# Optimization experiments

Hardware: AMD Instinct MI355X
Metric: run time of the kernel (lower is better)

## Reference

```python
import jax, jax.numpy as jnp
import numpy as np

B, N, D, H = 8, 2048, 512, 8  # batch, seq (incl. CLS), emb_dim, heads


def setup_inputs() -> dict:
    key = jax.random.key(0)
    kx, km, k1, k2, k3, k4 = jax.random.split(key, 6)
    x = jax.random.normal(kx, (B, N, D), dtype=jnp.float32)
    # mask covers the N-1 non-CLS tokens; forward pads a leading True for CLS
    mask = jax.random.bernoulli(km, p=0.9, shape=(B, N - 1))
    s = 0.02
    Wqkv = jax.random.normal(k1, (D, 3 * D), dtype=jnp.float32) * s
    bqkv = jax.random.normal(k2, (3 * D,), dtype=jnp.float32) * s
    Wout = jax.random.normal(k3, (D, D), dtype=jnp.float32) * s
    bout = jax.random.normal(k4, (D,), dtype=jnp.float32) * s
    return {"x": x, "mask": mask, "Wqkv": Wqkv, "bqkv": bqkv,
            "Wout": Wout, "bout": bout, "num_heads": H}


def reference(x, mask, Wqkv, bqkv, Wout, bout, num_heads):
    b, n, d = x.shape
    h = num_heads
    dh = d // h
    scale = d ** (-0.5)  # NOTE: module scales by emb_dim^-0.5, not head_dim^-0.5

    qkv = x @ Wqkv + bqkv                      # [b, n, 3d]
    q, k, v = jnp.split(qkv, 3, axis=-1)
    def to_heads(t):
        return t.reshape(b, n, h, dh).transpose(0, 2, 1, 3)  # [b, h, n, dh]
    q, k, v = map(to_heads, (q, k, v))

    scores = jnp.einsum('bhqd,bhkd->bhqk', q, k) * scale     # [b, h, n, n]

    # pad leading True for CLS token, then outer-product pair mask
    m = jnp.pad(mask, ((0, 0), (1, 0)), constant_values=True)  # [b, n]
    pair = m[:, None, :, None] & m[:, None, None, :]           # [b, 1, n, n]
    neg = jnp.asarray(-1e9, dtype=scores.dtype)  # finite stand-in for -inf (avoids NaN rows)
    scores = jnp.where(pair, scores, neg)

    attn = jax.nn.softmax(scores, axis=-1)
    out = jnp.einsum('bhqk,bhkd->bhqd', attn, v)               # [b, h, n, dh]
    out = out.transpose(0, 2, 1, 3).reshape(b, n, d)
    return out @ Wout + bout
```

## Files before the change

### kernel.cpp

```cpp
#include <hip/hip_runtime.h>
#include <math.h>

#define BB  8
#define SEQ 2048
#define EMB 512
#define NH  8
#define DH  64
#define NBH (BB * NH)
#define MROWS (BB * SEQ)
#define QKV_ELEMS ((size_t)NBH * SEQ * DH)
#define MASK_ELEMS (BB * (SEQ - 1))
#define QSCALE 0.06375871307545f

typedef __attribute__((ext_vector_type(8))) short short8;
typedef __attribute__((ext_vector_type(4))) float float4e;
typedef unsigned short ushort_t;

static __device__ inline unsigned short f2bf(float f) {
    unsigned int u = __float_as_uint(f);
    unsigned int r = (u + 0x7fffu + ((u >> 16) & 1u)) >> 16;
    return (unsigned short)r;
}

static __device__ inline float bf2f(unsigned short h) {
    return __uint_as_float((unsigned int)h << 16);
}

static __device__ inline void gl_lds16(const unsigned short* g, unsigned short* l) {
    __builtin_amdgcn_global_load_lds(
        (const __attribute__((address_space(1))) void*)g,
        (__attribute__((address_space(3))) void*)l, 16, 0, 0);
}

#define PREP_CONV   8192
#define PREP_MASK   (PREP_CONV + 64)
#define PREP_WQ     (PREP_MASK + (1536 / 32) * (EMB / 32))
#define PREP_TOTAL  (PREP_WQ + (EMB / 32) * (EMB / 32))

__global__ __launch_bounds__(256) void prep(const float* __restrict__ x,
                                            const void* __restrict__ mraw,
                                            const float* __restrict__ Wqkv,
                                            const float* __restrict__ Wout,
                                            ushort_t* __restrict__ xb,
                                            ushort_t* __restrict__ pmh,
                                            ushort_t* __restrict__ wqt,
                                            ushort_t* __restrict__ wot) {
    __shared__ float T[32][33];
    __shared__ int flag;
    const int bid = blockIdx.x;
    const int tid = threadIdx.x;

    if (bid < PREP_CONV) {
        const size_t i = ((size_t)bid * 256 + tid) * 4;
        float4 v = *(const float4*)&x[i];
        ushort4 o;
        o.x = f2bf(v.x); o.y = f2bf(v.y); o.z = f2bf(v.z); o.w = f2bf(v.w);
        *(ushort4*)&xb[i] = o;
    } else if (bid < PREP_MASK) {
        if (tid == 0) flag = 0;
        __syncthreads();
        const unsigned int* mi = (const unsigned int*)mraw;
        int local = 0;
        for (int i = tid; i < MASK_ELEMS / 4; i += 256) {
            if (mi[i] > 1u) local = 1;
        }
        if (local) flag = 1;
        __syncthreads();
        const int isbyte = flag;
        const unsigned char* mb = (const unsigned char*)mraw;
        const int* m32 = (const int*)mraw;
        const int i = (bid - PREP_CONV) * 256 + tid;
        const int b = i >> 11, n = i & (SEQ - 1);
        int v;
        if (n == 0) v = 1;
        else {
            const int src = b * (SEQ - 1) + n - 1;
            v = isbyte ? (int)mb[src] : (m32[src] != 0 ? 1 : 0);
        }
        pmh[i] = v ? 0x3F80 : 0;
    } else {
        const float* src;
        ushort_t* dst;
        int N, idx;
        if (bid < PREP_WQ) {
            src = Wqkv; dst = wqt; N = 1536; idx = bid - PREP_MASK;
        } else {
            src = Wout; dst = wot; N = EMB; idx = bid - PREP_WQ;
        }
        const int nb = N / 32;
        const int n0 = (idx % nb) * 32;
        const int k0 = (idx / nb) * 32;
        {
            const int r = tid >> 3, c4 = (tid & 7) * 4;
            *(float4*)&T[r][c4] = *(const float4*)&src[(size_t)(k0 + r) * N + n0 + c4];
        }
        __syncthreads();
        const int n = tid >> 3, k4 = (tid & 7) * 4;
        ushort4 hv;
        hv.x = f2bf(T[k4 + 0][n]);
        hv.y = f2bf(T[k4 + 1][n]);
        hv.z = f2bf(T[k4 + 2][n]);
        hv.w = f2bf(T[k4 + 3][n]);
        *(ushort4*)&dst[(size_t)(n0 + n) * EMB + k0 + k4] = hv;
    }
}

__global__ __launch_bounds__(256) void qkv_mfma(const ushort_t* __restrict__ xb,
                                                const ushort_t* __restrict__ wt,
                                                const float* __restrict__ bias,
                                                ushort_t* __restrict__ qb,
                                                ushort_t* __restrict__ kb,
                                                ushort_t* __restrict__ vt) {
    __shared__ __align__(16) ushort_t As[128 * 32];
    __shared__ __align__(16) ushort_t Bs[128 * 32];
    const int tid  = threadIdx.x;
    const int w    = tid >> 6;
    const int lane = tid & 63;
    const int l16  = lane & 15;
    const int quad = lane >> 4;
    const int wq   = w >> 1;
    const int wn   = w & 1;
    const int row0 = blockIdx.y * 128;
    const int col0 = blockIdx.x * 128;

    float4e acc[4][4];
    #pragma unroll
    for (int i = 0; i < 4; ++i)
        #pragma unroll
        for (int j = 0; j < 4; ++j) acc[i][j] = (float4e){0.f, 0.f, 0.f, 0.f};

    const int srow = tid >> 2;
    const int csrc = (tid & 3) ^ (srow & 3);

    for (int k0 = 0; k0 < EMB; k0 += 32) {
        #pragma unroll
        for (int s = 0; s < 2; ++s) {
            const int row = s * 64 + srow;
            gl_lds16(xb + (size_t)(row0 + row) * EMB + k0 + csrc * 8,
                     As + s * 2048 + w * 512);
            gl_lds16(wt + (size_t)(col0 + row) * EMB + k0 + csrc * 8,
                     Bs + s * 2048 + w * 512);
        }
        __syncthreads();
        short8 af[4], bf[4];
        #pragma unroll
        for (int mt = 0; mt < 4; ++mt) {
            const int rm = wq * 64 + mt * 16 + l16;
            af[mt] = *(const short8*)(As + rm * 32 + ((quad ^ (rm & 3)) * 8));
        }
        #pragma unroll
        for (int nt = 0; nt < 4; ++nt) {
            const int rn = wn * 64 + nt * 16 + l16;
            bf[nt] = *(const short8*)(Bs + rn * 32 + ((quad ^ (rn & 3)) * 8));
        }
        #pragma unroll
        for (int mt = 0; mt < 4; ++mt)
            #pragma unroll
            for (int nt = 0; nt < 4; ++nt)
                acc[mt][nt] = __builtin_amdgcn_mfma_f32_16x16x32_bf16(af[mt], bf[nt], acc[mt][nt], 0, 0, 0);
        __syncthreads();
    }

    #pragma unroll
    for (int nt = 0; nt < 4; ++nt) {
        const int cb    = col0 + wn * 64 + nt * 16;
        const int which = cb >> 9;
        const int h     = (cb >> 6) & 7;
        const int dcol  = (cb & 63) + l16;
        const float bz  = bias[cb + l16];
        if (which == 2) {
            #pragma unroll
            for (int mt = 0; mt < 4; ++mt) {
                const int rg = row0 + wq * 64 + mt * 16 + quad * 4;
                const int b = rg >> 11, n = rg & (SEQ - 1);
                ushort4 ov;
                ov.x = f2bf(acc[mt][nt][0] + bz);
                ov.y = f2bf(acc[mt][nt][1] + bz);
                ov.z = f2bf(acc[mt][nt][2] + bz);
                ov.w = f2bf(acc[mt][nt][3] + bz);
                *(ushort4*)&vt[((size_t)(b * NH + h) * DH + dcol) * SEQ + n] = ov;
            }
        } else {
            ushort_t* base = (which == 0) ? qb : kb;
            const float sc = (which == 0) ? QSCALE : 1.0f;
            #pragma unroll
            for (int mt = 0; mt < 4; ++mt) {
                #pragma unroll
                for (int i = 0; i < 4; ++i) {
                    const int rg = row0 + wq * 64 + mt * 16 + quad * 4 + i;
                    const int b = rg >> 11;
                    const int n = rg & (SEQ - 1);
                    base[((size_t)(b * NH + h) * SEQ + n) * DH + dcol] =
                        f2bf((acc[mt][nt][i] + bz) * sc);
                }
            }
        }
    }
}

__global__ __launch_bounds__(256, 4) void attn_mfma(const ushort_t* __restrict__ qb,
                                                    const ushort_t* __restrict__ kb,
                                                    const ushort_t* __restrict__ vt,
                                                    const ushort_t* __restrict__ pmh,
                                                    ushort_t* __restrict__ ab) {
    __shared__ __align__(16) ushort_t Ks[64 * 64];
    __shared__ __align__(16) ushort_t Vts[64 * 64];
    __shared__ __align__(16) ushort_t Ps[4][32 * 64];
    __shared__ ushort_t mskh[SEQ];
    __shared__ float lw[128];

    const int tid  = threadIdx.x;
    const int qt   = blockIdx.x & 15;
    const int bh   = blockIdx.x >> 4;
    const int b    = bh >> 3;
    const int h    = bh & 7;
    const int w    = tid >> 6;
    const int lane = tid & 63;
    const int l16  = lane & 15;
    const int quad = lane >> 4;

    *(short8*)(mskh + tid * 8) = *(const short8*)(pmh + b * SEQ + tid * 8);

    const ushort_t* qbase = qb + ((size_t)bh * SEQ + qt * 128 + w * 32 + l16) * DH;
    short8 qf0[2], qf1[2];
    #pragma unroll
    for (int g = 0; g < 2; ++g) {
        qf0[g] = *(const short8*)(qbase + g * 16 * DH + quad * 8);
        qf1[g] = *(const short8*)(qbase + g * 16 * DH + 32 + quad * 8);
    }

    float mqf[2], fnq[2];
    #pragma unroll
    for (int g = 0; g < 2; ++g) {
        mqf[g] = bf2f(pmh[b * SEQ + qt * 128 + w * 32 + g * 16 + l16]);
        fnq[g] = 1.0f - mqf[g];
    }

    float4e o[2][4];
    #pragma unroll
    for (int g = 0; g < 2; ++g)
        #pragma unroll
        for (int d = 0; d < 4; ++d) o[g][d] = (float4e){0.f, 0.f, 0.f, 0.f};
    float l_i[2] = {0.f, 0.f};

    int crow[2], ccol[2], cdst[2];
    #pragma unroll
    for (int s = 0; s < 2; ++s) {
        const int c = s * 256 + tid;
        crow[s] = c >> 3;
        ccol[s] = (c & 7) * 8;
        cdst[s] = crow[s] * 64 + (((c & 7) ^ (crow[s] & 7)) * 8);
    }
    const ushort_t* kptr = kb + (size_t)bh * SEQ * DH;
    const ushort_t* vptr = vt + (size_t)bh * DH * SEQ;

    int koff0[4], koff1[4];
    #pragma unroll
    for (int t = 0; t < 4; ++t) {
        const int row = t * 16 + l16;
        koff0[t] = row * 64 + ((quad ^ (row & 7)) * 8);
        koff1[t] = row * 64 + (((4 + quad) ^ (row & 7)) * 8);
    }
    const int psw = (l16 & 7) * 2;
    ushort_t* pwv = &Ps[w][0];
    const int prd0 = ((quad * 2) ^ psw) * 4;
    const int prd1 = (((4 + quad) * 2) ^ psw) * 4;

    short8 kreg[2], vreg[2];
    #pragma unroll
    for (int s = 0; s < 2; ++s) {
        kreg[s] = *(const short8*)(kptr + (size_t)crow[s] * DH + ccol[s]);
        vreg[s] = *(const short8*)(vptr + (size_t)crow[s] * SEQ + ccol[s]);
    }

    for (int kt = 0; kt < 32; ++kt) {
        __syncthreads();
        #pragma unroll
        for (int s = 0; s < 2; ++s) {
            *(short8*)(Ks + cdst[s])  = kreg[s];
            *(short8*)(Vts + cdst[s]) = vreg[s];
        }
        __syncthreads();

        if (kt < 31) {
            #pragma unroll
            for (int s = 0; s < 2; ++s) {
                kreg[s] = *(const short8*)(kptr + (size_t)((kt + 1) * 64 + crow[s]) * DH + ccol[s]);
                vreg[s] = *(const short8*)(vptr + (size_t)crow[s] * SEQ + (kt + 1) * 64 + ccol[s]);
            }
        }

        #pragma unroll
        for (int bkb = 0; bkb < 4; ++bkb) {
            const short8 kf0 = *(const short8*)(Ks + koff0[bkb]);
            const short8 kf1 = *(const short8*)(Ks + koff1[bkb]);
            float4e st[2];
            #pragma unroll
            for (int g = 0; g < 2; ++g) {
                st[g] = (float4e){0.f, 0.f, 0.f, 0.f};
                st[g] = __builtin_amdgcn_mfma_f32_16x16x32_bf16(kf0, qf0[g], st[g], 0, 0, 0);
                st[g] = __builtin_amdgcn_mfma_f32_16x16x32_bf16(kf1, qf1[g], st[g], 0, 0, 0);
            }
            const ushort4 mk4 = *(const ushort4*)(mskh + kt * 64 + bkb * 16 + quad * 4);
            const float mkf[4] = {bf2f(mk4.x), bf2f(mk4.y), bf2f(mk4.z), bf2f(mk4.w)};
            const int pc = ((bkb * 4 + quad) ^ psw) * 4;
            #pragma unroll
            for (int g = 0; g < 2; ++g) {
                float p0 = fmaf(__builtin_amdgcn_exp2f(st[g][0]) * mkf[0], mqf[g], fnq[g]);
                float p1 = fmaf(__builtin_amdgcn_exp2f(st[g][1]) * mkf[1], mqf[g], fnq[g]);
                float p2 = fmaf(__builtin_amdgcn_exp2f(st[g][2]) * mkf[2], mqf[g], fnq[g]);
                float p3 = fmaf(__builtin_amdgcn_exp2f(st[g][3]) * mkf[3], mqf[g], fnq[g]);
                l_i[g] += (p0 + p1) + (p2 + p3);
                ushort4 pk;
                pk.x = f2bf(p0); pk.y = f2bf(p1); pk.z = f2bf(p2); pk.w = f2bf(p3);
                *(ushort4*)(pwv + (g * 16 + l16) * 64 + pc) = pk;
            }
        }

        short8 pf0[2], pf1[2];
        #pragma unroll
        for (int g = 0; g < 2; ++g) {
            pf0[g] = *(const short8*)(pwv + (g * 16 + l16) * 64 + prd0);
            pf1[g] = *(const short8*)(pwv + (g * 16 + l16) * 64 + prd1);
        }
        #pragma unroll
        for (int dhb = 0; dhb < 4; ++dhb) {
            const short8 vf0 = *(const short8*)(Vts + koff0[dhb]);
            const short8 vf1 = *(const short8*)(Vts + koff1[dhb]);
            #pragma unroll
            for (int g = 0; g < 2; ++g) {
                o[g][dhb] = __builtin_amdgcn_mfma_f32_16x16x32_bf16(pf0[g], vf0, o[g][dhb], 0, 0, 0);
                o[g][dhb] = __builtin_amdgcn_mfma_f32_16x16x32_bf16(pf1[g], vf1, o[g][dhb], 0, 0, 0);
            }
        }
    }

    #pragma unroll
    for (int g = 0; g < 2; ++g) {
        float l = l_i[g];
        l += __shfl_xor(l, 16);
        l += __shfl_xor(l, 32);
        lw[w * 32 + g * 16 + l16] = l;
    }

    ushort_t* ob = ab + ((size_t)b * SEQ + qt * 128 + w * 32) * EMB + h * DH;
    #pragma unroll
    for (int g = 0; g < 2; ++g) {
        #pragma unroll
        for (int i = 0; i < 4; ++i) {
            const int row = g * 16 + quad * 4 + i;
            const float inv = 1.0f / lw[w * 32 + row];
            #pragma unroll
            for (int dhb = 0; dhb < 4; ++dhb)
                ob[(size_t)row * EMB + dhb * 16 + l16] = f2bf(o[g][dhb][i] * inv);
        }
    }
}

__global__ __launch_bounds__(256) void out_mfma(const ushort_t* __restrict__ ab,
                                                const ushort_t* __restrict__ wot,
                                                const float* __restrict__ bias,
                                                float* __restrict__ out) {
    __shared__ __align__(16) ushort_t As[128 * 32];
    __shared__ __align__(16) ushort_t Bs[128 * 32];
    const int tid  = threadIdx.x;
    const int w    = tid >> 6;
    const int lane = tid & 63;
    const int l16  = lane & 15;
    const int quad = lane >> 4;
    const int wq   = w >> 1;
    const int wn   = w & 1;
    const int row0 = blockIdx.y * 128;
    const int col0 = blockIdx.x * 128;

    float4e acc[4][4];
    #pragma unroll
    for (int i = 0; i < 4; ++i)
        #pragma unroll
        for (int j = 0; j < 4; ++j) acc[i][j] = (float4e){0.f, 0.f, 0.f, 0.f};

    const int srow = tid >> 2;
    const int csrc = (tid & 3) ^ (srow & 3);

    for (int k0 = 0; k0 < EMB; k0 += 32) {
        #pragma unroll
        for (int s = 0; s < 2; ++s) {
            const int row = s * 64 + srow;
            gl_lds16(ab + (size_t)(row0 + row) * EMB + k0 + csrc * 8,
                     As + s * 2048 + w * 512);
            gl_lds16(wot + (size_t)(col0 + row) * EMB + k0 + csrc * 8,
                     Bs + s * 2048 + w * 512);
        }
        __syncthreads();
        short8 af[4], bf[4];
        #pragma unroll
        for (int mt = 0; mt < 4; ++mt) {
            const int rm = wq * 64 + mt * 16 + l16;
            af[mt] = *(const short8*)(As + rm * 32 + ((quad ^ (rm & 3)) * 8));
        }
        #pragma unroll
        for (int nt = 0; nt < 4; ++nt) {
            const int rn = wn * 64 + nt * 16 + l16;
            bf[nt] = *(const short8*)(Bs + rn * 32 + ((quad ^ (rn & 3)) * 8));
        }
        #pragma unroll
        for (int mt = 0; mt < 4; ++mt)
            #pragma unroll
            for (int nt = 0; nt < 4; ++nt)
                acc[mt][nt] = __builtin_amdgcn_mfma_f32_16x16x32_bf16(af[mt], bf[nt], acc[mt][nt], 0, 0, 0);
        __syncthreads();
    }

    #pragma unroll
    for (int nt = 0; nt < 4; ++nt) {
        const int col_g = col0 + wn * 64 + nt * 16 + l16;
        const float bz = bias[col_g];
        #pragma unroll
        for (int mt = 0; mt < 4; ++mt) {
            #pragma unroll
            for (int i = 0; i < 4; ++i) {
                const int row_g = row0 + wq * 64 + mt * 16 + quad * 4 + i;
                out[(size_t)row_g * EMB + col_g] = acc[mt][nt][i] + bz;
            }
        }
    }
}

extern "C" void kernel_launch(void* const* d_in, const int* in_sizes, int n_in,
                              void* d_out, int out_size, void* d_ws, size_t ws_size,
                              hipStream_t stream) {
    const float* x    = (const float*)d_in[0];
    const void*  mask = d_in[1];
    const float* Wqkv = (const float*)d_in[2];
    const float* bqkv = (const float*)d_in[3];
    const float* Wout = (const float*)d_in[4];
    const float* bout = (const float*)d_in[5];
    float* out = (float*)d_out;

    ushort_t* xb  = (ushort_t*)d_ws;
    ushort_t* wqt = xb + (size_t)MROWS * EMB;
    ushort_t* wot = wqt + (size_t)1536 * EMB;
    ushort_t* qb  = wot + (size_t)EMB * EMB;
    ushort_t* kb  = qb + QKV_ELEMS;
    ushort_t* vt  = kb + QKV_ELEMS;
    ushort_t* ab  = vt + QKV_ELEMS;
    ushort_t* pmh = ab + (size_t)MROWS * EMB;

    prep<<<dim3(PREP_TOTAL), 256, 0, stream>>>(x, mask, Wqkv, Wout, xb, pmh, wqt, wot);
    qkv_mfma<<<dim3(1536 / 128, MROWS / 128), 256, 0, stream>>>(xb, wqt, bqkv, qb, kb, vt);
    attn_mfma<<<dim3(NBH * (SEQ / 128)), 256, 0, stream>>>(qb, kb, vt, pmh, ab);
    out_mfma<<<dim3(EMB / 128, MROWS / 128), 256, 0, stream>>>(ab, wot, bout, out);
}
```

Baseline: 280.0 us.

## Rewrite attention with 32x32 MFMA, register-resident P, async double-buffered K/V staging

The attention kernel moves from 16x16x32 to 32x32x16 bf16 MFMA, with 2 waves of 64 query rows each instead of 4 waves of 32. Probabilities stay in registers and are repacked with cross-half-wave shuffles instead of going through LDS. K/V tiles are double-buffered with direct global-to-LDS loads, which drops one barrier per iteration. The mask becomes float and is read from global/cache rather than staged in LDS. P is truncated rather than rounded to bf16, and the smaller 128-thread blocks may cut latency hiding.

```diff
diff --git a/kernel.cpp b/kernel.cpp
--- a/kernel.cpp
+++ b/kernel.cpp
@@ -12,18 +12,16 @@
 #define MASK_ELEMS (BB * (SEQ - 1))
 #define QSCALE 0.06375871307545f
 
-typedef __attribute__((ext_vector_type(8))) short short8;
-typedef __attribute__((ext_vector_type(4))) float float4e;
+typedef __attribute__((ext_vector_type(8)))  short short8;
+typedef __attribute__((ext_vector_type(4)))  float float4e;
+typedef __attribute__((ext_vector_type(16))) float float16e;
+typedef __attribute__((ext_vector_type(4)))  unsigned int uint4e;
 typedef unsigned short ushort_t;
 
 static __device__ inline unsigned short f2bf(float f) {
     unsigned int u = __float_as_uint(f);
     unsigned int r = (u + 0x7fffu + ((u >> 16) & 1u)) >> 16;
     return (unsigned short)r;
-}
-
-static __device__ inline float bf2f(unsigned short h) {
-    return __uint_as_float((unsigned int)h << 16);
 }
 
 static __device__ inline void gl_lds16(const unsigned short* g, unsigned short* l) {
@@ -42,7 +40,7 @@
                                             const float* __restrict__ Wqkv,
                                             const float* __restrict__ Wout,
                                             ushort_t* __restrict__ xb,
-                                            ushort_t* __restrict__ pmh,
+                                            float* __restrict__ pmf,
                                             ushort_t* __restrict__ wqt,
                                             ushort_t* __restrict__ wot) {
     __shared__ float T[32][33];
@@ -77,7 +75,7 @@
             const int src = b * (SEQ - 1) + n - 1;
             v = isbyte ? (int)mb[src] : (m32[src] != 0 ? 1 : 0);
         }
-        pmh[i] = v ? 0x3F80 : 0;
+        pmf[i] = v ? 1.0f : 0.0f;
     } else {
         const float* src;
         ushort_t* dst;
@@ -198,161 +196,161 @@
     }
 }
 
-__global__ __launch_bounds__(256, 4) void attn_mfma(const ushort_t* __restrict__ qb,
+__device__ inline void stage_tile(const ushort_t* kbh, const ushort_t* vbh, int kt,
+                                  ushort_t* Kd, ushort_t* Vd,
+                                  const int* crow, const int* csoff, int wbase) {
+    #pragma unroll
+    for (int j = 0; j < 4; ++j) {
+        gl_lds16(kbh + (size_t)(kt * 64 + crow[j]) * DH + csoff[j],
+                 Kd + (j * 128 + wbase) * 8);
+        gl_lds16(vbh + (size_t)crow[j] * SEQ + kt * 64 + csoff[j],
+                 Vd + (j * 128 + wbase) * 8);
+    }
+}
+
+__global__ __launch_bounds__(128, 2) void attn_mfma(const ushort_t* __restrict__ qb,
                                                     const ushort_t* __restrict__ kb,
                                                     const ushort_t* __restrict__ vt,
-                                                    const ushort_t* __restrict__ pmh,
+                                                    const float* __restrict__ pmf,
                                                     ushort_t* __restrict__ ab) {
-    __shared__ __align__(16) ushort_t Ks[64 * 64];
-    __shared__ __align__(16) ushort_t Vts[64 * 64];
-    __shared__ __align__(16) ushort_t Ps[4][32 * 64];
-    __shared__ ushort_t mskh[SEQ];
-    __shared__ float lw[128];
-
-    const int tid  = threadIdx.x;
-    const int qt   = blockIdx.x & 15;
-    const int bh   = blockIdx.x >> 4;
-    const int b    = bh >> 3;
-    const int h    = bh & 7;
-    const int w    = tid >> 6;
+    __shared__ __align__(16) ushort_t Ks[2][64 * 64];
+    __shared__ __align__(16) ushort_t Vts[2][64 * 64];
+    __shared__ float lw[2][64];
+
+    const int tid = threadIdx.x;
+    const int w   = tid >> 6;
     const int lane = tid & 63;
-    const int l16  = lane & 15;
-    const int quad = lane >> 4;
-
-    *(short8*)(mskh + tid * 8) = *(const short8*)(pmh + b * SEQ + tid * 8);
-
-    const ushort_t* qbase = qb + ((size_t)bh * SEQ + qt * 128 + w * 32 + l16) * DH;
-    short8 qf0[2], qf1[2];
-    #pragma unroll
-    for (int g = 0; g < 2; ++g) {
-        qf0[g] = *(const short8*)(qbase + g * 16 * DH + quad * 8);
-        qf1[g] = *(const short8*)(qbase + g * 16 * DH + 32 + quad * 8);
-    }
-
-    float mqf[2], fnq[2];
-    #pragma unroll
-    for (int g = 0; g < 2; ++g) {
-        mqf[g] = bf2f(pmh[b * SEQ + qt * 128 + w * 32 + g * 16 + l16]);
-        fnq[g] = 1.0f - mqf[g];
-    }
-
-    float4e o[2][4];
-    #pragma unroll
-    for (int g = 0; g < 2; ++g)
-        #pragma unroll
-        for (int d = 0; d < 4; ++d) o[g][d] = (float4e){0.f, 0.f, 0.f, 0.f};
+    const int l5  = lane & 31;
+    const int h   = lane >> 5;
+    const int qt  = blockIdx.x & 15;
+    const int bh  = blockIdx.x >> 4;
+    const int b   = bh >> 3;
+    const int hh  = bh & 7;
+    const int q0  = qt * 128 + w * 64;
+
+    const ushort_t* qbh = qb + (size_t)bh * SEQ * DH;
+    short8 qf[2][4];
+    #pragma unroll
+    for (int t = 0; t < 2; ++t)
+        #pragma unroll
+        for (int kc = 0; kc < 4; ++kc)
+            qf[t][kc] = *(const short8*)(qbh + (size_t)(q0 + t * 32 + l5) * DH + kc * 16 + h * 8);
+
+    float mq[2], fnq[2];
+    #pragma unroll
+    for (int t = 0; t < 2; ++t) {
+        mq[t]  = pmf[b * SEQ + q0 + t * 32 + l5];
+        fnq[t] = 1.0f - mq[t];
+    }
+
+    int crow[4], csoff[4];
+    #pragma unroll
+    for (int j = 0; j < 4; ++j) {
+        const int c = j * 128 + tid;
+        crow[j]  = c >> 3;
+        csoff[j] = ((c & 7) ^ (crow[j] & 7)) * 8;
+    }
+    const int wbase = w * 64;
+    const ushort_t* kbh = kb + (size_t)bh * SEQ * DH;
+    const ushort_t* vbh = vt + (size_t)bh * DH * SEQ;
+    const float*    mrow = pmf + b * SEQ;
+
+    float16e o[2][2];
+    #pragma unroll
+    for (int t = 0; t < 2; ++t)
+        #pragma unroll
+        for (int d = 0; d < 2; ++d) o[t][d] = (float16e)0.0f;
     float l_i[2] = {0.f, 0.f};
 
-    int crow[2], ccol[2], cdst[2];
-    #pragma unroll
-    for (int s = 0; s < 2; ++s) {
-        const int c = s * 256 + tid;
-        crow[s] = c >> 3;
-        ccol[s] = (c & 7) * 8;
-        cdst[s] = crow[s] * 64 + (((c & 7) ^ (crow[s] & 7)) * 8);
-    }
-    const ushort_t* kptr = kb + (size_t)bh * SEQ * DH;
-    const ushort_t* vptr = vt + (size_t)bh * DH * SEQ;
-
-    int koff0[4], koff1[4];
-    #pragma unroll
-    for (int t = 0; t < 4; ++t) {
-        const int row = t * 16 + l16;
-        koff0[t] = row * 64 + ((quad ^ (row & 7)) * 8);
-        koff1[t] = row * 64 + (((4 + quad) ^ (row & 7)) * 8);
-    }
-    const int psw = (l16 & 7) * 2;
-    ushort_t* pwv = &Ps[w][0];
-    const int prd0 = ((quad * 2) ^ psw) * 4;
-    const int prd1 = (((4 + quad) * 2) ^ psw) * 4;
-
-    short8 kreg[2], vreg[2];
-    #pragma unroll
-    for (int s = 0; s < 2; ++s) {
-        kreg[s] = *(const short8*)(kptr + (size_t)crow[s] * DH + ccol[s]);
-        vreg[s] = *(const short8*)(vptr + (size_t)crow[s] * SEQ + ccol[s]);
-    }
+    stage_tile(kbh, vbh, 0, Ks[0], Vts[0], crow, csoff, wbase);
 
     for (int kt = 0; kt < 32; ++kt) {
         __syncthreads();
+        const int cur = kt & 1;
+        if (kt < 31)
+            stage_tile(kbh, vbh, kt + 1, Ks[cur ^ 1], Vts[cur ^ 1], crow, csoff, wbase);
+
         #pragma unroll
         for (int s = 0; s < 2; ++s) {
-            *(short8*)(Ks + cdst[s])  = kreg[s];
-            *(short8*)(Vts + cdst[s]) = vreg[s];
-        }
-        __syncthreads();
-
-        if (kt < 31) {
-            #pragma unroll
-            for (int s = 0; s < 2; ++s) {
-                kreg[s] = *(const short8*)(kptr + (size_t)((kt + 1) * 64 + crow[s]) * DH + ccol[s]);
-                vreg[s] = *(const short8*)(vptr + (size_t)crow[s] * SEQ + (kt + 1) * 64 + ccol[s]);
-            }
-        }
-
-        #pragma unroll
-        for (int bkb = 0; bkb < 4; ++bkb) {
-            const short8 kf0 = *(const short8*)(Ks + koff0[bkb]);
-            const short8 kf1 = *(const short8*)(Ks + koff1[bkb]);
-            float4e st[2];
-            #pragma unroll
-            for (int g = 0; g < 2; ++g) {
-                st[g] = (float4e){0.f, 0.f, 0.f, 0.f};
-                st[g] = __builtin_amdgcn_mfma_f32_16x16x32_bf16(kf0, qf0[g], st[g], 0, 0, 0);
-                st[g] = __builtin_amdgcn_mfma_f32_16x16x32_bf16(kf1, qf1[g], st[g], 0, 0, 0);
-            }
-            const ushort4 mk4 = *(const ushort4*)(mskh + kt * 64 + bkb * 16 + quad * 4);
-            const float mkf[4] = {bf2f(mk4.x), bf2f(mk4.y), bf2f(mk4.z), bf2f(mk4.w)};
-            const int pc = ((bkb * 4 + quad) ^ psw) * 4;
-            #pragma unroll
-            for (int g = 0; g < 2; ++g) {
-                float p0 = fmaf(__builtin_amdgcn_exp2f(st[g][0]) * mkf[0], mqf[g], fnq[g]);
-                float p1 = fmaf(__builtin_amdgcn_exp2f(st[g][1]) * mkf[1], mqf[g], fnq[g]);
-                float p2 = fmaf(__builtin_amdgcn_exp2f(st[g][2]) * mkf[2], mqf[g], fnq[g]);
-                float p3 = fmaf(__builtin_amdgcn_exp2f(st[g][3]) * mkf[3], mqf[g], fnq[g]);
-                l_i[g] += (p0 + p1) + (p2 + p3);
-                ushort4 pk;
-                pk.x = f2bf(p0); pk.y = f2bf(p1); pk.z = f2bf(p2); pk.w = f2bf(p3);
-                *(ushort4*)(pwv + (g * 16 + l16) * 64 + pc) = pk;
-            }
-        }
-
-        short8 pf0[2], pf1[2];
-        #pragma unroll
-        for (int g = 0; g < 2; ++g) {
-            pf0[g] = *(const short8*)(pwv + (g * 16 + l16) * 64 + prd0);
-            pf1[g] = *(const short8*)(pwv + (g * 16 + l16) * 64 + prd1);
-        }
-        #pragma unroll
-        for (int dhb = 0; dhb < 4; ++dhb) {
-            const short8 vf0 = *(const short8*)(Vts + koff0[dhb]);
-            const short8 vf1 = *(const short8*)(Vts + koff1[dhb]);
-            #pragma unroll
-            for (int g = 0; g < 2; ++g) {
-                o[g][dhb] = __builtin_amdgcn_mfma_f32_16x16x32_bf16(pf0[g], vf0, o[g][dhb], 0, 0, 0);
-                o[g][dhb] = __builtin_amdgcn_mfma_f32_16x16x32_bf16(pf1[g], vf1, o[g][dhb], 0, 0, 0);
-            }
-        }
-    }
-
-    #pragma unroll
-    for (int g = 0; g < 2; ++g) {
-        float l = l_i[g];
-        l += __shfl_xor(l, 16);
-        l += __shfl_xor(l, 32);
-        lw[w * 32 + g * 16 + l16] = l;
-    }
-
-    ushort_t* ob = ab + ((size_t)b * SEQ + qt * 128 + w * 32) * EMB + h * DH;
-    #pragma unroll
-    for (int g = 0; g < 2; ++g) {
-        #pragma unroll
-        for (int i = 0; i < 4; ++i) {
-            const int row = g * 16 + quad * 4 + i;
-            const float inv = 1.0f / lw[w * 32 + row];
-            #pragma unroll
-            for (int dhb = 0; dhb < 4; ++dhb)
-                ob[(size_t)row * EMB + dhb * 16 + l16] = f2bf(o[g][dhb][i] * inv);
+            const int krow = s * 32 + l5;
+            short8 kf[4];
+            #pragma unroll
+            for (int kc = 0; kc < 4; ++kc)
+                kf[kc] = *(const short8*)(Ks[cur] + krow * 64 + (((kc * 2 + h) ^ (krow & 7)) * 8));
+            float16e st[2];
+            st[0] = (float16e)0.0f;
+            st[1] = (float16e)0.0f;
+            #pragma unroll
+            for (int kc = 0; kc < 4; ++kc) {
+                st[0] = __builtin_amdgcn_mfma_f32_32x32x16_bf16(kf[kc], qf[0][kc], st[0], 0, 0, 0);
+                st[1] = __builtin_amdgcn_mfma_f32_32x32x16_bf16(kf[kc], qf[1][kc], st[1], 0, 0, 0);
+            }
+
+            float4e mk4[4];
+            #pragma unroll
+            for (int g2 = 0; g2 < 4; ++g2)
+                mk4[g2] = *(const float4e*)(mrow + kt * 64 + s * 32 + g2 * 8 + h * 4);
+
+            short8 af[2][2];
+            #pragma unroll
+            for (int t = 0; t < 2; ++t) {
+                unsigned int a[8];
+                float lacc = 0.f;
+                #pragma unroll
+                for (int j = 0; j < 8; ++j) {
+                    const float mk0 = mk4[j >> 1][(2 * j) & 3];
+                    const float mk1 = mk4[j >> 1][(2 * j + 1) & 3];
+                    const float p0 = fmaf(__builtin_amdgcn_exp2f(st[t][2 * j]) * mk0, mq[t], fnq[t]);
+                    const float p1 = fmaf(__builtin_amdgcn_exp2f(st[t][2 * j + 1]) * mk1, mq[t], fnq[t]);
+                    lacc += p0 + p1;
+                    a[j] = (__float_as_uint(p0) >> 16) | (__float_as_uint(p1) & 0xffff0000u);
+                }
+                l_i[t] += lacc;
+                #pragma unroll
+                for (int c = 0; c < 2; ++c) {
+                    const unsigned int s0 = h ? a[4 * c]     : a[4 * c + 2];
+                    const unsigned int s1 = h ? a[4 * c + 1] : a[4 * c + 3];
+                    const unsigned int x0 = (unsigned int)__shfl_xor((int)s0, 32);
+                    const unsigned int x1 = (unsigned int)__shfl_xor((int)s1, 32);
+                    uint4e fv;
+                    fv.x = h ? x0 : a[4 * c];
+                    fv.y = h ? x1 : a[4 * c + 1];
+                    fv.z = h ? a[4 * c + 2] : x0;
+                    fv.w = h ? a[4 * c + 3] : x1;
+                    af[t][c] = __builtin_bit_cast(short8, fv);
+                }
+            }
+
+            #pragma unroll
+            for (int c = 0; c < 2; ++c) {
+                #pragma unroll
+                for (int d = 0; d < 2; ++d) {
+                    const int vrow = d * 32 + l5;
+                    const short8 vf = *(const short8*)(Vts[cur] + vrow * 64 +
+                                       (((s * 4 + c * 2 + h) ^ (vrow & 7)) * 8));
+                    o[0][d] = __builtin_amdgcn_mfma_f32_32x32x16_bf16(af[0][c], vf, o[0][d], 0, 0, 0);
+                    o[1][d] = __builtin_amdgcn_mfma_f32_32x32x16_bf16(af[1][c], vf, o[1][d], 0, 0, 0);
+                }
+            }
+        }
+    }
+
+    #pragma unroll
+    for (int t = 0; t < 2; ++t) {
+        const float l = l_i[t] + __shfl_xor(l_i[t], 32);
+        lw[w][t * 32 + l5] = l;
+    }
+
+    ushort_t* ob = ab + ((size_t)b * SEQ + q0) * EMB + hh * DH;
+    #pragma unroll
+    for (int t = 0; t < 2; ++t) {
+        #pragma unroll
+        for (int r = 0; r < 16; ++r) {
+            const int ql = (r & 3) + 8 * (r >> 2) + 4 * h;
+            const float inv = 1.0f / lw[w][t * 32 + ql];
+            #pragma unroll
+            for (int d = 0; d < 2; ++d)
+                ob[(size_t)(t * 32 + ql) * EMB + d * 32 + l5] = f2bf(o[t][d][r] * inv);
         }
     }
 }
@@ -444,10 +442,10 @@
     ushort_t* kb  = qb + QKV_ELEMS;
     ushort_t* vt  = kb + QKV_ELEMS;
     ushort_t* ab  = vt + QKV_ELEMS;
-    ushort_t* pmh = ab + (size_t)MROWS * EMB;
-
-    prep<<<dim3(PREP_TOTAL), 256, 0, stream>>>(x, mask, Wqkv, Wout, xb, pmh, wqt, wot);
+    float*    pmf = (float*)(ab + (size_t)MROWS * EMB);
+
+    prep<<<dim3(PREP_TOTAL), 256, 0, stream>>>(x, mask, Wqkv, Wout, xb, pmf, wqt, wot);
     qkv_mfma<<<dim3(1536 / 128, MROWS / 128), 256, 0, stream>>>(xb, wqt, bqkv, qb, kb, vt);
-    attn_mfma<<<dim3(NBH * (SEQ / 128)), 256, 0, stream>>>(qb, kb, vt, pmh, ab);
+    attn_mfma<<<dim3(NBH * (SEQ / 128)), 128, 0, stream>>>(qb, kb, vt, pmf, ab);
     out_mfma<<<dim3(EMB / 128, MROWS / 128), 256, 0, stream>>>(ab, wot, bout, out);
 }
```

After: 255.3 us. 8.8% less time.
